# Kernel optimization log

Hardware: AMD Instinct MI355X
Metric: run time of the kernel (lower is better)

The kernel has to match this reference:

```python
import jax, jax.numpy as jnp
import numpy as np

B, S, D, H, E, K = 4, 4096, 256, 1024, 8, 2


def setup_inputs() -> dict:
    key = jax.random.key(0)
    ks = jax.random.split(key, 7)
    sc = 0.02
    return {
        "x": jax.random.normal(ks[0], (B, S, D), dtype=jnp.float32),
        "w_router": jax.random.normal(ks[1], (D, E), dtype=jnp.float32) * sc,
        "b_router": jnp.zeros((E,), dtype=jnp.float32),
        "w1": jax.random.normal(ks[2], (E, D, H), dtype=jnp.float32) * sc,
        "b1": jnp.zeros((E, H), dtype=jnp.float32),
        "w2": jax.random.normal(ks[3], (E, H, D), dtype=jnp.float32) * sc,
        "b2": jnp.zeros((E, D), dtype=jnp.float32),
    }


def reference(x, w_router, b_router, w1, b1, w2, b2):
    # Router: softmax over experts, then top-k selection + renormalization
    router_logits = jnp.einsum("bsd,de->bse", x, w_router) + b_router
    router_probs = jax.nn.softmax(router_logits, axis=-1)            # [B,S,E]
    top_probs, top_idx = jax.lax.top_k(router_probs, K)               # [B,S,K]
    top_w = top_probs / jnp.sum(top_probs, axis=-1, keepdims=True)    # renorm

    # Combine weights per expert: sum_k one_hot(idx_k) * w_k  -> [B,S,E]
    combine = jnp.sum(jax.nn.one_hot(top_idx, E, dtype=x.dtype) * top_w[..., None], axis=-2)

    # Dense equivalent of the masked gather/scatter dispatch:
    # out[b,s] = sum_e combine[b,s,e] * Expert_e(x[b,s])
    h = jax.nn.gelu(jnp.einsum("bsd,edh->bseh", x, w1) + b1, approximate=False)  # [B,S,E,H]
    y = jnp.einsum("bseh,ehd->bsed", h, w2) + b2                                  # [B,S,E,D]
    out = jnp.einsum("bsed,bse->bsd", y, combine)                                  # [B,S,D]
    return out, router_probs
```

## Files before the change

kernel.cpp:

```cpp
#include <hip/hip_runtime.h>

typedef float f32x4 __attribute__((ext_vector_type(4)));
typedef short s16x8 __attribute__((ext_vector_type(8)));

static constexpr int NTOK = 16384;
static constexpr int D    = 256;
static constexpr int H    = 1024;
static constexpr int E    = 8;

__device__ __forceinline__ float bf2f(unsigned short u) {
    return __uint_as_float(((unsigned int)u) << 16);
}
__device__ __forceinline__ unsigned short f2bf(float f) {
    unsigned int u = __float_as_uint(f);
    u += 0x7FFFu + ((u >> 16) & 1u);
    return (unsigned short)(u >> 16);
}
__device__ __forceinline__ s16x8 pack8(float4 a, float4 b) {
    s16x8 v;
    v[0] = (short)f2bf(a.x); v[1] = (short)f2bf(a.y);
    v[2] = (short)f2bf(a.z); v[3] = (short)f2bf(a.w);
    v[4] = (short)f2bf(b.x); v[5] = (short)f2bf(b.y);
    v[6] = (short)f2bf(b.z); v[7] = (short)f2bf(b.w);
    return v;
}

__global__ void __launch_bounds__(256) convert_kernel(
    const float* __restrict__ w1, const float* __restrict__ w2,
    unsigned short* __restrict__ w1t, unsigned short* __restrict__ w2t)
{
    __shared__ unsigned short tile[32][33];
    int b = blockIdx.x;
    const float* src; unsigned short* dst;
    int Rr, Cc, tr, tc;
    if (b < 2048) {
        int e = b >> 8, tt = b & 255;
        Rr = 256; Cc = 1024; tr = tt >> 5; tc = tt & 31;
        src = w1 + (size_t)e * Rr * Cc; dst = w1t + (size_t)e * Rr * Cc;
    } else {
        b -= 2048;
        int e = b >> 8, tt = b & 255;
        Rr = 1024; Cc = 256; tr = tt >> 3; tc = tt & 7;
        src = w2 + (size_t)e * Rr * Cc; dst = w2t + (size_t)e * Rr * Cc;
    }
    const int tid = threadIdx.x;
    const int c = tid & 31, r0 = tid >> 5;
    #pragma unroll
    for (int rr = 0; rr < 32; rr += 8)
        tile[r0 + rr][c] = f2bf(src[(size_t)(tr * 32 + r0 + rr) * Cc + tc * 32 + c]);
    __syncthreads();
    #pragma unroll
    for (int rr = 0; rr < 32; rr += 8)
        dst[(size_t)(tc * 32 + r0 + rr) * Rr + tr * 32 + c] = tile[c][r0 + rr];
}

__global__ void __launch_bounds__(1024) router_kernel(
    const float* __restrict__ x,
    const float* __restrict__ wr,
    const float* __restrict__ br,
    float* __restrict__ probs_out,
    int* __restrict__ cnt, int* __restrict__ list, float* __restrict__ wlist)
{
    __shared__ float wrs[D][9];
    __shared__ int lcnt[8];
    __shared__ int gbase[8];
    const int tid = threadIdx.x;
    if (tid < 256) {
        float4 a = *reinterpret_cast<const float4*>(wr + tid * 8);
        float4 b = *reinterpret_cast<const float4*>(wr + tid * 8 + 4);
        wrs[tid][0] = a.x; wrs[tid][1] = a.y; wrs[tid][2] = a.z; wrs[tid][3] = a.w;
        wrs[tid][4] = b.x; wrs[tid][5] = b.y; wrs[tid][6] = b.z; wrs[tid][7] = b.w;
    }
    if (tid < 8) lcnt[tid] = 0;
    __syncthreads();

    const int g = tid >> 4, l = tid & 15;
    const int t = blockIdx.x * 64 + g;

    float lg[8];
    #pragma unroll
    for (int e = 0; e < 8; ++e) lg[e] = 0.f;

    const float* xr = x + (size_t)t * D;
    #pragma unroll
    for (int r = 0; r < 4; ++r) {
        const int d = r * 64 + l * 4;
        float4 xv = *reinterpret_cast<const float4*>(xr + d);
        #pragma unroll
        for (int j = 0; j < 4; ++j) {
            const float xf = (j == 0) ? xv.x : (j == 1) ? xv.y : (j == 2) ? xv.z : xv.w;
            #pragma unroll
            for (int e = 0; e < 8; ++e) lg[e] += xf * wrs[d + j][e];
        }
    }
    #pragma unroll
    for (int off = 1; off < 16; off <<= 1)
        #pragma unroll
        for (int e = 0; e < 8; ++e) lg[e] += __shfl_xor(lg[e], off, 16);

    int i1 = 0, i2 = 0, lp1 = 0, lp2 = 0;
    float wa = 0.f, wb = 0.f;
    if (l == 0) {
        #pragma unroll
        for (int e = 0; e < 8; ++e) lg[e] += br[e];
        float mx = lg[0];
        #pragma unroll
        for (int e = 1; e < 8; ++e) mx = fmaxf(mx, lg[e]);
        float p[8], s = 0.f;
        #pragma unroll
        for (int e = 0; e < 8; ++e) { p[e] = expf(lg[e] - mx); s += p[e]; }
        const float inv = 1.f / s;
        #pragma unroll
        for (int e = 0; e < 8; ++e) p[e] *= inv;
        float4 o0 = {p[0], p[1], p[2], p[3]}, o1 = {p[4], p[5], p[6], p[7]};
        *reinterpret_cast<float4*>(probs_out + t * 8)     = o0;
        *reinterpret_cast<float4*>(probs_out + t * 8 + 4) = o1;

        #pragma unroll
        for (int e = 1; e < 8; ++e) if (p[e] > p[i1]) i1 = e;
        i2 = (i1 == 0) ? 1 : 0;
        #pragma unroll
        for (int e = 0; e < 8; ++e) if (e != i1 && p[e] > p[i2]) i2 = e;
        const float sw = p[i1] + p[i2];
        wa = p[i1] / sw; wb = p[i2] / sw;
        lp1 = atomicAdd(&lcnt[i1], 1);
        lp2 = atomicAdd(&lcnt[i2], 1);
    }
    __syncthreads();
    if (tid < 8) gbase[tid] = atomicAdd(&cnt[tid], lcnt[tid]);
    __syncthreads();
    if (l == 0) {
        int pos = gbase[i1] + lp1;
        list[i1 * NTOK + pos] = t;
        wlist[i1 * NTOK + pos] = wa;
        pos = gbase[i2] + lp2;
        list[i2 * NTOK + pos] = t | (1 << 30);
        wlist[i2 * NTOK + pos] = wb;
    }
}

__global__ void __launch_bounds__(512, 4) expert_kernel_v5(
    const float* __restrict__ x,
    const unsigned short* __restrict__ w1t,
    const unsigned short* __restrict__ w2t,
    const float* __restrict__ b1,
    const float* __restrict__ b2,
    const int* __restrict__ cnt, const int* __restrict__ list,
    const float* __restrict__ wlist,
    float* __restrict__ out,
    float* __restrict__ ybuf32,
    unsigned short* __restrict__ ybuf16,
    const int mode)
{
    const int e = blockIdx.y;
    int n = cnt[e]; n = (n < 0) ? 0 : ((n > NTOK) ? NTOK : n);
    const int tile0 = blockIdx.x * 64;
    if (tile0 >= n) return;
    const int nvalid = (n - tile0 < 64) ? (n - tile0) : 64;

    __shared__ __align__(16) unsigned short W1s[2][32 * 264];
    __shared__ __align__(16) unsigned short W2s[2][256 * 32];
    __shared__ __align__(16) unsigned short Hs [2][64 * 40];
    __shared__ int   toks[64];
    __shared__ float wgts[64];

    const int tid  = threadIdx.x;
    const int lane = tid & 63;
    const int wv   = tid >> 6;
    const int mrow = lane & 15;
    const int kb   = lane >> 4;
    const int key4 = (mrow & 3) ^ ((mrow >> 2) & 3);
    const int rb    = wv & 3;
    const int chb   = wv >> 2;
    const int tpart = wv & 1;
    const int dpart = wv >> 1;

    if (tid < 64) {
        if (tid < nvalid) {
            toks[tid] = list[e * NTOK + tile0 + tid];
            wgts[tid] = wlist[e * NTOK + tile0 + tid];
        } else { toks[tid] = 0; wgts[tid] = 0.f; }
    }

    const size_t w1b = (size_t)e * H * D;
    const size_t w2b = (size_t)e * D * H;
    s16x8 pfW1[2], pfW2[2];

    #define LOADW1(HC)                                                                  \
        _Pragma("unroll")                                                               \
        for (int k = 0; k < 2; ++k) {                                                   \
            const int s = k * 512 + tid, h1 = s >> 5, c1 = s & 31;                      \
            pfW1[k] = *reinterpret_cast<const s16x8*>(                                  \
                w1t + w1b + (size_t)((HC) * 32 + h1) * D + c1 * 8);                     \
        }
    #define STOREW1(BUF)                                                                \
        _Pragma("unroll")                                                               \
        for (int k = 0; k < 2; ++k) {                                                   \
            const int s = k * 512 + tid, h1 = s >> 5, c1 = s & 31;                      \
            *reinterpret_cast<s16x8*>(&W1s[BUF][h1 * 264 + c1 * 8]) = pfW1[k];          \
        }
    #define LOADW2(HC)                                                                  \
        _Pragma("unroll")                                                               \
        for (int k = 0; k < 2; ++k) {                                                   \
            const int s = k * 512 + tid, d2 = s >> 2, c2 = s & 3;                       \
            pfW2[k] = *reinterpret_cast<const s16x8*>(                                  \
                w2t + w2b + (size_t)d2 * H + (HC) * 32 + c2 * 8);                       \
        }
    #define STOREW2(BUF)                                                                \
        _Pragma("unroll")                                                               \
        for (int k = 0; k < 2; ++k) {                                                   \
            const int s = k * 512 + tid, d2 = s >> 2, c2 = s & 3;                       \
            const int k2 = (d2 & 3) ^ ((d2 >> 2) & 3);                                  \
            *reinterpret_cast<s16x8*>(&W2s[BUF][d2 * 32 + ((c2 ^ k2) << 3)]) = pfW2[k]; \
        }

    LOADW1(0);
    __syncthreads();

    s16x8 aFrag[8];
    {
        const float* xrow = x + (size_t)(toks[rb * 16 + mrow] & 0x3FFF) * D;
        #pragma unroll
        for (int ks = 0; ks < 8; ++ks) {
            const float* src = xrow + ks * 32 + kb * 8;
            aFrag[ks] = pack8(*reinterpret_cast<const float4*>(src),
                              *reinterpret_cast<const float4*>(src + 4));
        }
    }

    STOREW1(0);
    LOADW1(1);
    LOADW2(0);
    __syncthreads();

    f32x4 accYt[2][4];
    #pragma unroll
    for (int i = 0; i < 2; ++i)
        #pragma unroll
        for (int j = 0; j < 4; ++j) accYt[i][j] = (f32x4){0.f, 0.f, 0.f, 0.f};

    for (int hc = 0; hc < 32; ++hc) {
        const int cur = hc & 1, nxt = cur ^ 1;

        if (hc < 31) { STOREW1(nxt); }
        if (hc < 30) { LOADW1(hc + 2); }
        STOREW2(cur);
        if (hc < 31) { LOADW2(hc + 1); }

        f32x4 accH = (f32x4){0.f, 0.f, 0.f, 0.f};
        {
            const int brow = chb * 16 + mrow;
            #pragma unroll
            for (int ks = 0; ks < 8; ++ks) {
                s16x8 bfrag = *reinterpret_cast<const s16x8*>(
                    &W1s[cur][brow * 264 + ks * 32 + kb * 8]);
                accH = __builtin_amdgcn_mfma_f32_16x16x32_bf16(aFrag[ks], bfrag, accH, 0, 0, 0);
            }
            const float bias = b1[e * H + hc * 32 + brow];
            #pragma unroll
            for (int r = 0; r < 4; ++r) {
                const int t = rb * 16 + kb * 4 + r;
                const float vvf = accH[r] + bias;
                const float g = 0.5f * vvf * (1.0f + erff(vvf * 0.70710678118654752f));
                Hs[cur][t * 40 + brow] = f2bf(g);
            }
        }

        if (hc > 0) {
            s16x8 bfrag[2];
            #pragma unroll
            for (int tg = 0; tg < 2; ++tg)
                bfrag[tg] = *reinterpret_cast<const s16x8*>(
                    &Hs[nxt][((tpart * 2 + tg) * 16 + mrow) * 40 + kb * 8]);
            #pragma unroll
            for (int db = 0; db < 4; ++db) {
                const int d = (dpart * 4 + db) * 16 + mrow;
                s16x8 afrag = *reinterpret_cast<const s16x8*>(
                    &W2s[nxt][d * 32 + ((kb ^ key4) << 3)]);
                #pragma unroll
                for (int tg = 0; tg < 2; ++tg)
                    accYt[tg][db] = __builtin_amdgcn_mfma_f32_16x16x32_bf16(
                        afrag, bfrag[tg], accYt[tg][db], 0, 0, 0);
            }
        }
        __syncthreads();
    }

    {
        s16x8 bfrag[2];
        #pragma unroll
        for (int tg = 0; tg < 2; ++tg)
            bfrag[tg] = *reinterpret_cast<const s16x8*>(
                &Hs[1][((tpart * 2 + tg) * 16 + mrow) * 40 + kb * 8]);
        #pragma unroll
        for (int db = 0; db < 4; ++db) {
            const int d = (dpart * 4 + db) * 16 + mrow;
            s16x8 afrag = *reinterpret_cast<const s16x8*>(
                &W2s[1][d * 32 + ((kb ^ key4) << 3)]);
            #pragma unroll
            for (int tg = 0; tg < 2; ++tg)
                accYt[tg][db] = __builtin_amdgcn_mfma_f32_16x16x32_bf16(
                    afrag, bfrag[tg], accYt[tg][db], 0, 0, 0);
        }
    }

    #pragma unroll
    for (int tg = 0; tg < 2; ++tg) {
        const int tloc = (tpart * 2 + tg) * 16 + mrow;
        if (tloc < nvalid) {
            const float wt = wgts[tloc];
            const int raw = toks[tloc];
            const int t = raw & 0x3FFF;
            const size_t slotbase = ((size_t)((raw >> 30) & 1) * NTOK + t) * D;
            if (mode == 1) {
                float* ybase = ybuf32 + slotbase;
                #pragma unroll
                for (int db = 0; db < 4; ++db) {
                    const int d0 = (dpart * 4 + db) * 16 + kb * 4;
                    const float4 bv = *reinterpret_cast<const float4*>(b2 + e * D + d0);
                    float4 v = {(accYt[tg][db][0] + bv.x) * wt, (accYt[tg][db][1] + bv.y) * wt,
                                (accYt[tg][db][2] + bv.z) * wt, (accYt[tg][db][3] + bv.w) * wt};
                    *reinterpret_cast<float4*>(ybase + d0) = v;
                }
            } else if (mode == 2) {
                unsigned short* ybase = ybuf16 + slotbase;
                #pragma unroll
                for (int db = 0; db < 4; ++db) {
                    const int d0 = (dpart * 4 + db) * 16 + kb * 4;
                    const float4 bv = *reinterpret_cast<const float4*>(b2 + e * D + d0);
                    ushort4 v;
                    v.x = f2bf((accYt[tg][db][0] + bv.x) * wt);
                    v.y = f2bf((accYt[tg][db][1] + bv.y) * wt);
                    v.z = f2bf((accYt[tg][db][2] + bv.z) * wt);
                    v.w = f2bf((accYt[tg][db][3] + bv.w) * wt);
                    *reinterpret_cast<ushort4*>(ybase + d0) = v;
                }
            } else {
                float* obase = out + (size_t)t * D;
                #pragma unroll
                for (int db = 0; db < 4; ++db) {
                    const int d0 = (dpart * 4 + db) * 16 + kb * 4;
                    const float4 bv = *reinterpret_cast<const float4*>(b2 + e * D + d0);
                    atomicAdd(obase + d0 + 0, (accYt[tg][db][0] + bv.x) * wt);
                    atomicAdd(obase + d0 + 1, (accYt[tg][db][1] + bv.y) * wt);
                    atomicAdd(obase + d0 + 2, (accYt[tg][db][2] + bv.z) * wt);
                    atomicAdd(obase + d0 + 3, (accYt[tg][db][3] + bv.w) * wt);
                }
            }
        }
    }
    #undef LOADW1
    #undef STOREW1
    #undef LOADW2
    #undef STOREW2
}

__global__ void __launch_bounds__(256) combine_f32_kernel(
    const float* __restrict__ ybuf, float* __restrict__ out)
{
    const size_t i = ((size_t)blockIdx.x * 256 + threadIdx.x) * 4;
    float4 a = *reinterpret_cast<const float4*>(ybuf + i);
    float4 b = *reinterpret_cast<const float4*>(ybuf + (size_t)NTOK * D + i);
    float4 v = {a.x + b.x, a.y + b.y, a.z + b.z, a.w + b.w};
    *reinterpret_cast<float4*>(out + i) = v;
}
__global__ void __launch_bounds__(256) combine_bf16_kernel(
    const unsigned short* __restrict__ ybuf, float* __restrict__ out)
{
    const size_t i = ((size_t)blockIdx.x * 256 + threadIdx.x) * 4;
    ushort4 a = *reinterpret_cast<const ushort4*>(ybuf + i);
    ushort4 b = *reinterpret_cast<const ushort4*>(ybuf + (size_t)NTOK * D + i);
    float4 v = {bf2f(a.x) + bf2f(b.x), bf2f(a.y) + bf2f(b.y),
                bf2f(a.z) + bf2f(b.z), bf2f(a.w) + bf2f(b.w)};
    *reinterpret_cast<float4*>(out + i) = v;
}

__global__ void __launch_bounds__(256) expert_kernel_fp32(
    const float* __restrict__ x, const float* __restrict__ w1, const float* __restrict__ w2,
    const float* __restrict__ b1, const float* __restrict__ b2,
    const int* __restrict__ cnt, const int* __restrict__ list, const float* __restrict__ wlist,
    float* __restrict__ out)
{
    const int e = blockIdx.y;
    int n = cnt[e]; n = (n < 0) ? 0 : ((n > NTOK) ? NTOK : n);
    const int tile0 = blockIdx.x * 64;
    if (tile0 >= n) return;
    const int nvalid = (n - tile0 < 64) ? (n - tile0) : 64;

    __shared__ __align__(16) unsigned short Xs [64 * 264];
    __shared__ __align__(16) unsigned short W1s[64 * 264];
    __shared__ __align__(16) unsigned short W2s[256 * 72];
    __shared__ __align__(16) unsigned short Hs [64 * 72];
    __shared__ int   toks[64];
    __shared__ float wgts[64];

    const int tid = threadIdx.x, lane = tid & 63, wv = tid >> 6;
    const int mrow = lane & 15, kb = lane >> 4;

    if (tid < 64) {
        if (tid < nvalid) {
            toks[tid] = list[e * NTOK + tile0 + tid] & 0x3FFF;
            wgts[tid] = wlist[e * NTOK + tile0 + tid];
        } else { toks[tid] = 0; wgts[tid] = 0.f; }
    }
    __syncthreads();

    #pragma unroll
    for (int r = 0; r < 8; ++r) {
        int v = r * 256 + tid, row = v >> 5, c8 = v & 31;
        s16x8 val = {0,0,0,0,0,0,0,0};
        if (row < nvalid) {
            const float* src = x + (size_t)toks[row] * D + c8 * 8;
            val = pack8(*reinterpret_cast<const float4*>(src),
                        *reinterpret_cast<const float4*>(src + 4));
        }
        *reinterpret_cast<s16x8*>(&Xs[row * 264 + c8 * 8]) = val;
    }

    f32x4 accYt[16];
    #pragma unroll
    for (int i = 0; i < 16; ++i) accYt[i] = (f32x4){0.f, 0.f, 0.f, 0.f};

    const int wr2 = wv >> 1, wc2 = wv & 1;
    const int hgrp = tid & 7, dblk = tid >> 3;
    const int dgrp = tid & 31, hblk8 = tid >> 5;

    for (int hc = 0; hc < 16; ++hc) {
        __syncthreads();
        {
            s16x8 Y8[8];
            #pragma unroll
            for (int i = 0; i < 8; ++i) {
                const float* src = w1 + ((size_t)(e * D + dblk * 8 + i)) * H + hc * 64 + hgrp * 8;
                Y8[i] = pack8(*reinterpret_cast<const float4*>(src),
                              *reinterpret_cast<const float4*>(src + 4));
            }
            #pragma unroll
            for (int j = 0; j < 8; ++j) {
                s16x8 V;
                #pragma unroll
                for (int i = 0; i < 8; ++i) V[i] = Y8[i][j];
                *reinterpret_cast<s16x8*>(&W1s[(hgrp * 8 + j) * 264 + dblk * 8]) = V;
            }
        }
        {
            s16x8 Z8[8];
            #pragma unroll
            for (int i = 0; i < 8; ++i) {
                const float* src = w2 + ((size_t)(e * H + hc * 64 + hblk8 * 8 + i)) * D + dgrp * 8;
                Z8[i] = pack8(*reinterpret_cast<const float4*>(src),
                              *reinterpret_cast<const float4*>(src + 4));
            }
            const int hswz = (hblk8 ^ (dgrp & 7)) << 3;
            #pragma unroll
            for (int j = 0; j < 8; ++j) {
                s16x8 V;
                #pragma unroll
                for (int i = 0; i < 8; ++i) V[i] = Z8[i][j];
                *reinterpret_cast<s16x8*>(&W2s[(dgrp * 8 + j) * 72 + hswz]) = V;
            }
        }
        __syncthreads();

        f32x4 accH[2][2];
        #pragma unroll
        for (int i = 0; i < 2; ++i)
            #pragma unroll
            for (int j = 0; j < 2; ++j) accH[i][j] = (f32x4){0.f, 0.f, 0.f, 0.f};
        #pragma unroll
        for (int ks = 0; ks < 8; ++ks) {
            const int koff = ks * 32 + kb * 8;
            s16x8 a0 = *reinterpret_cast<const s16x8*>(&Xs [((wr2*2+0)*16 + mrow)*264 + koff]);
            s16x8 a1 = *reinterpret_cast<const s16x8*>(&Xs [((wr2*2+1)*16 + mrow)*264 + koff]);
            s16x8 b0 = *reinterpret_cast<const s16x8*>(&W1s[((wc2*2+0)*16 + mrow)*264 + koff]);
            s16x8 b1v= *reinterpret_cast<const s16x8*>(&W1s[((wc2*2+1)*16 + mrow)*264 + koff]);
            accH[0][0] = __builtin_amdgcn_mfma_f32_16x16x32_bf16(a0, b0,  accH[0][0], 0, 0, 0);
            accH[0][1] = __builtin_amdgcn_mfma_f32_16x16x32_bf16(a0, b1v, accH[0][1], 0, 0, 0);
            accH[1][0] = __builtin_amdgcn_mfma_f32_16x16x32_bf16(a1, b0,  accH[1][0], 0, 0, 0);
            accH[1][1] = __builtin_amdgcn_mfma_f32_16x16x32_bf16(a1, b1v, accH[1][1], 0, 0, 0);
        }
        #pragma unroll
        for (int i = 0; i < 2; ++i)
            #pragma unroll
            for (int j = 0; j < 2; ++j) {
                const int hloc = (wc2*2 + j) * 16 + mrow;
                const float bias = b1[e * H + hc * 64 + hloc];
                #pragma unroll
                for (int r = 0; r < 4; ++r) {
                    const int m = (wr2*2 + i) * 16 + kb * 4 + r;
                    float vvf = accH[i][j][r] + bias;
                    float g = 0.5f * vvf * (1.0f + erff(vvf * 0.70710678118654752f));
                    Hs[m * 72 + hloc] = f2bf(g);
                }
            }
        __syncthreads();

        #pragma unroll
        for (int ks = 0; ks < 2; ++ks) {
            const int koff = ks * 32 + kb * 8;
            s16x8 bfrag = *reinterpret_cast<const s16x8*>(&Hs[(wv * 16 + mrow) * 72 + koff]);
            #pragma unroll
            for (int db = 0; db < 16; ++db) {
                const int arow = db * 16 + mrow;
                const int akey = (arow >> 3) & 7;
                s16x8 afrag = *reinterpret_cast<const s16x8*>(
                    &W2s[arow * 72 + (((ks * 4 + kb) ^ akey) << 3)]);
                accYt[db] = __builtin_amdgcn_mfma_f32_16x16x32_bf16(afrag, bfrag, accYt[db], 0, 0, 0);
            }
        }
    }

    {
        const int t = wv * 16 + mrow;
        if (t < nvalid) {
            const float wt = wgts[t];
            float* obase = out + (size_t)toks[t] * D;
            #pragma unroll
            for (int db = 0; db < 16; ++db) {
                const int d0 = db * 16 + kb * 4;
                #pragma unroll
                for (int r = 0; r < 4; ++r)
                    atomicAdd(obase + d0 + r, (accYt[db][r] + b2[e * D + d0 + r]) * wt);
            }
        }
    }
}

extern "C" void kernel_launch(void* const* d_in, const int* in_sizes, int n_in,
                              void* d_out, int out_size, void* d_ws, size_t ws_size,
                              hipStream_t stream)
{
    const float* x  = (const float*)d_in[0];
    const float* wr = (const float*)d_in[1];
    const float* br = (const float*)d_in[2];
    const float* w1 = (const float*)d_in[3];
    const float* b1 = (const float*)d_in[4];
    const float* w2 = (const float*)d_in[5];
    const float* b2 = (const float*)d_in[6];
    float* out = (float*)d_out;

    char* ws = (char*)d_ws;
    int*   cnt   = (int*)ws;
    int*   list  = (int*)(ws + 256);
    float* wlist = (float*)(ws + 524544);
    unsigned short* w1t = (unsigned short*)(ws + 1048832);
    unsigned short* w2t = (unsigned short*)(ws + 5243136);
    float*          ybuf32 = (float*)(ws + 9437440);
    unsigned short* ybuf16 = (unsigned short*)(ws + 9437440);

    const bool big = ws_size >= 9437440;
    int mode = 0;
    if (big) {
        if (ws_size >= 9437440ull + 33554432ull)      mode = 1;
        else if (ws_size >= 9437440ull + 16777216ull) mode = 2;
    }

    if (mode == 0)
        hipMemsetAsync(out, 0, (size_t)NTOK * D * 4, stream);
    hipMemsetAsync(cnt, 0, 256, stream);
    if (big)
        convert_kernel<<<4096, 256, 0, stream>>>(w1, w2, w1t, w2t);
    router_kernel<<<NTOK / 64, 1024, 0, stream>>>(x, wr, br, out + (size_t)NTOK * D, cnt, list, wlist);
    if (big) {
        expert_kernel_v5<<<dim3(256, 8), 512, 0, stream>>>(
            x, w1t, w2t, b1, b2, cnt, list, wlist, out, ybuf32, ybuf16, mode);
        if (mode == 1)
            combine_f32_kernel<<<(NTOK * D / 4) / 256, 256, 0, stream>>>(ybuf32, out);
        else if (mode == 2)
            combine_bf16_kernel<<<(NTOK * D / 4) / 256, 256, 0, stream>>>(ybuf16, out);
    } else {
        expert_kernel_fp32<<<dim3(256, 8), 256, 0, stream>>>(x, w1, w2, b1, b2, cnt, list, wlist, out);
    }
}
```

Baseline: 219.4 us.

## Fuse weight conversion with router, use tanh GELU approximation, lighter barrier

Merges the weight transpose/convert kernel and the router kernel into one launch, with block ranges split by blockIdx, so one kernel launch and its dependency gap go away. Replaces the exact erf GELU in the expert kernel with a tanh-form approximation built from __expf and a fast divide, which cuts transcendental cost but changes numerics relative to the exact-GELU reference. Swaps the per-iteration __syncthreads for a barrier that waits only on LDS counters, so outstanding global loads can stay in flight across the barrier. In the non-big fallback path the prep kernel also runs the conversion blocks, writing into w1t/w2t pointers that may not fit in the workspace.

```diff
diff --git a/kernel.cpp b/kernel.cpp
--- a/kernel.cpp
+++ b/kernel.cpp
@@ -25,121 +25,125 @@
     return v;
 }
 
-__global__ void __launch_bounds__(256) convert_kernel(
+__device__ __forceinline__ void barrier_lds_only() {
+    __asm__ __volatile__("s_waitcnt lgkmcnt(0)" ::: "memory");
+    __builtin_amdgcn_s_barrier();
+    __asm__ __volatile__("" ::: "memory");
+}
+
+__global__ void __launch_bounds__(256) prep_kernel(
     const float* __restrict__ w1, const float* __restrict__ w2,
-    unsigned short* __restrict__ w1t, unsigned short* __restrict__ w2t)
-{
-    __shared__ unsigned short tile[32][33];
-    int b = blockIdx.x;
-    const float* src; unsigned short* dst;
-    int Rr, Cc, tr, tc;
-    if (b < 2048) {
-        int e = b >> 8, tt = b & 255;
-        Rr = 256; Cc = 1024; tr = tt >> 5; tc = tt & 31;
-        src = w1 + (size_t)e * Rr * Cc; dst = w1t + (size_t)e * Rr * Cc;
-    } else {
-        b -= 2048;
-        int e = b >> 8, tt = b & 255;
-        Rr = 1024; Cc = 256; tr = tt >> 3; tc = tt & 7;
-        src = w2 + (size_t)e * Rr * Cc; dst = w2t + (size_t)e * Rr * Cc;
-    }
-    const int tid = threadIdx.x;
-    const int c = tid & 31, r0 = tid >> 5;
-    #pragma unroll
-    for (int rr = 0; rr < 32; rr += 8)
-        tile[r0 + rr][c] = f2bf(src[(size_t)(tr * 32 + r0 + rr) * Cc + tc * 32 + c]);
-    __syncthreads();
-    #pragma unroll
-    for (int rr = 0; rr < 32; rr += 8)
-        dst[(size_t)(tc * 32 + r0 + rr) * Rr + tr * 32 + c] = tile[c][r0 + rr];
-}
-
-__global__ void __launch_bounds__(1024) router_kernel(
-    const float* __restrict__ x,
-    const float* __restrict__ wr,
-    const float* __restrict__ br,
-    float* __restrict__ probs_out,
+    unsigned short* __restrict__ w1t, unsigned short* __restrict__ w2t,
+    const float* __restrict__ x, const float* __restrict__ wr,
+    const float* __restrict__ br, float* __restrict__ probs_out,
     int* __restrict__ cnt, int* __restrict__ list, float* __restrict__ wlist)
 {
-    __shared__ float wrs[D][9];
-    __shared__ int lcnt[8];
-    __shared__ int gbase[8];
+    __shared__ __align__(16) char smem[9280];
     const int tid = threadIdx.x;
-    if (tid < 256) {
-        float4 a = *reinterpret_cast<const float4*>(wr + tid * 8);
-        float4 b = *reinterpret_cast<const float4*>(wr + tid * 8 + 4);
-        wrs[tid][0] = a.x; wrs[tid][1] = a.y; wrs[tid][2] = a.z; wrs[tid][3] = a.w;
-        wrs[tid][4] = b.x; wrs[tid][5] = b.y; wrs[tid][6] = b.z; wrs[tid][7] = b.w;
-    }
-    if (tid < 8) lcnt[tid] = 0;
-    __syncthreads();
-
-    const int g = tid >> 4, l = tid & 15;
-    const int t = blockIdx.x * 64 + g;
-
-    float lg[8];
-    #pragma unroll
-    for (int e = 0; e < 8; ++e) lg[e] = 0.f;
-
-    const float* xr = x + (size_t)t * D;
-    #pragma unroll
-    for (int r = 0; r < 4; ++r) {
-        const int d = r * 64 + l * 4;
-        float4 xv = *reinterpret_cast<const float4*>(xr + d);
-        #pragma unroll
-        for (int j = 0; j < 4; ++j) {
-            const float xf = (j == 0) ? xv.x : (j == 1) ? xv.y : (j == 2) ? xv.z : xv.w;
-            #pragma unroll
-            for (int e = 0; e < 8; ++e) lg[e] += xf * wrs[d + j][e];
-        }
-    }
-    #pragma unroll
-    for (int off = 1; off < 16; off <<= 1)
-        #pragma unroll
-        for (int e = 0; e < 8; ++e) lg[e] += __shfl_xor(lg[e], off, 16);
-
-    int i1 = 0, i2 = 0, lp1 = 0, lp2 = 0;
-    float wa = 0.f, wb = 0.f;
-    if (l == 0) {
-        #pragma unroll
-        for (int e = 0; e < 8; ++e) lg[e] += br[e];
-        float mx = lg[0];
-        #pragma unroll
-        for (int e = 1; e < 8; ++e) mx = fmaxf(mx, lg[e]);
-        float p[8], s = 0.f;
-        #pragma unroll
-        for (int e = 0; e < 8; ++e) { p[e] = expf(lg[e] - mx); s += p[e]; }
-        const float inv = 1.f / s;
-        #pragma unroll
-        for (int e = 0; e < 8; ++e) p[e] *= inv;
-        float4 o0 = {p[0], p[1], p[2], p[3]}, o1 = {p[4], p[5], p[6], p[7]};
-        *reinterpret_cast<float4*>(probs_out + t * 8)     = o0;
-        *reinterpret_cast<float4*>(probs_out + t * 8 + 4) = o1;
-
-        #pragma unroll
-        for (int e = 1; e < 8; ++e) if (p[e] > p[i1]) i1 = e;
-        i2 = (i1 == 0) ? 1 : 0;
-        #pragma unroll
-        for (int e = 0; e < 8; ++e) if (e != i1 && p[e] > p[i2]) i2 = e;
-        const float sw = p[i1] + p[i2];
-        wa = p[i1] / sw; wb = p[i2] / sw;
-        lp1 = atomicAdd(&lcnt[i1], 1);
-        lp2 = atomicAdd(&lcnt[i2], 1);
-    }
-    __syncthreads();
-    if (tid < 8) gbase[tid] = atomicAdd(&cnt[tid], lcnt[tid]);
-    __syncthreads();
-    if (l == 0) {
-        int pos = gbase[i1] + lp1;
-        list[i1 * NTOK + pos] = t;
-        wlist[i1 * NTOK + pos] = wa;
-        pos = gbase[i2] + lp2;
-        list[i2 * NTOK + pos] = t | (1 << 30);
-        wlist[i2 * NTOK + pos] = wb;
-    }
-}
-
-__global__ void __launch_bounds__(512, 4) expert_kernel_v5(
+
+    if (blockIdx.x < 4096) {
+        unsigned short (*tile)[33] = reinterpret_cast<unsigned short(*)[33]>(smem);
+        int b = blockIdx.x;
+        const float* src; unsigned short* dst;
+        int Rr, Cc, tr, tc;
+        if (b < 2048) {
+            int e = b >> 8, tt = b & 255;
+            Rr = 256; Cc = 1024; tr = tt >> 5; tc = tt & 31;
+            src = w1 + (size_t)e * Rr * Cc; dst = w1t + (size_t)e * Rr * Cc;
+        } else {
+            b -= 2048;
+            int e = b >> 8, tt = b & 255;
+            Rr = 1024; Cc = 256; tr = tt >> 3; tc = tt & 7;
+            src = w2 + (size_t)e * Rr * Cc; dst = w2t + (size_t)e * Rr * Cc;
+        }
+        const int c = tid & 31, r0 = tid >> 5;
+        #pragma unroll
+        for (int rr = 0; rr < 32; rr += 8)
+            tile[r0 + rr][c] = f2bf(src[(size_t)(tr * 32 + r0 + rr) * Cc + tc * 32 + c]);
+        __syncthreads();
+        #pragma unroll
+        for (int rr = 0; rr < 32; rr += 8)
+            dst[(size_t)(tc * 32 + r0 + rr) * Rr + tr * 32 + c] = tile[c][r0 + rr];
+    } else {
+        float (*wrs)[9] = reinterpret_cast<float(*)[9]>(smem);
+        int* lcnt  = reinterpret_cast<int*>(smem + 9216);
+        int* gbase = lcnt + 8;
+
+        if (tid < 8) lcnt[tid] = 0;
+        {
+            float4 a = *reinterpret_cast<const float4*>(wr + tid * 8);
+            float4 b = *reinterpret_cast<const float4*>(wr + tid * 8 + 4);
+            wrs[tid][0] = a.x; wrs[tid][1] = a.y; wrs[tid][2] = a.z; wrs[tid][3] = a.w;
+            wrs[tid][4] = b.x; wrs[tid][5] = b.y; wrs[tid][6] = b.z; wrs[tid][7] = b.w;
+        }
+        __syncthreads();
+
+        const int g = tid >> 4, l = tid & 15;
+        const int t = (blockIdx.x - 4096) * 16 + g;
+
+        float lg[8];
+        #pragma unroll
+        for (int e = 0; e < 8; ++e) lg[e] = 0.f;
+        const float* xr = x + (size_t)t * D;
+        #pragma unroll
+        for (int r = 0; r < 4; ++r) {
+            const int d = r * 64 + l * 4;
+            float4 xv = *reinterpret_cast<const float4*>(xr + d);
+            #pragma unroll
+            for (int j = 0; j < 4; ++j) {
+                const float xf = (j == 0) ? xv.x : (j == 1) ? xv.y : (j == 2) ? xv.z : xv.w;
+                #pragma unroll
+                for (int e = 0; e < 8; ++e) lg[e] += xf * wrs[d + j][e];
+            }
+        }
+        #pragma unroll
+        for (int off = 1; off < 16; off <<= 1)
+            #pragma unroll
+            for (int e = 0; e < 8; ++e) lg[e] += __shfl_xor(lg[e], off, 16);
+
+        int i1 = 0, i2 = 0, lp1 = 0, lp2 = 0;
+        float wa = 0.f, wb = 0.f;
+        if (l == 0) {
+            #pragma unroll
+            for (int e = 0; e < 8; ++e) lg[e] += br[e];
+            float mx = lg[0];
+            #pragma unroll
+            for (int e = 1; e < 8; ++e) mx = fmaxf(mx, lg[e]);
+            float p[8], s = 0.f;
+            #pragma unroll
+            for (int e = 0; e < 8; ++e) { p[e] = expf(lg[e] - mx); s += p[e]; }
+            const float inv = 1.f / s;
+            #pragma unroll
+            for (int e = 0; e < 8; ++e) p[e] *= inv;
+            float4 o0 = {p[0], p[1], p[2], p[3]}, o1 = {p[4], p[5], p[6], p[7]};
+            *reinterpret_cast<float4*>(probs_out + t * 8)     = o0;
+            *reinterpret_cast<float4*>(probs_out + t * 8 + 4) = o1;
+
+            #pragma unroll
+            for (int e = 1; e < 8; ++e) if (p[e] > p[i1]) i1 = e;
+            i2 = (i1 == 0) ? 1 : 0;
+            #pragma unroll
+            for (int e = 0; e < 8; ++e) if (e != i1 && p[e] > p[i2]) i2 = e;
+            const float sw = p[i1] + p[i2];
+            wa = p[i1] / sw; wb = p[i2] / sw;
+            lp1 = atomicAdd(&lcnt[i1], 1);
+            lp2 = atomicAdd(&lcnt[i2], 1);
+        }
+        __syncthreads();
+        if (tid < 8) gbase[tid] = atomicAdd(&cnt[tid], lcnt[tid]);
+        __syncthreads();
+        if (l == 0) {
+            int pos = gbase[i1] + lp1;
+            list[i1 * NTOK + pos] = t;
+            wlist[i1 * NTOK + pos] = wa;
+            pos = gbase[i2] + lp2;
+            list[i2 * NTOK + pos] = t | (1 << 30);
+            wlist[i2 * NTOK + pos] = wb;
+        }
+    }
+}
+
+__global__ void __launch_bounds__(512, 4) expert_kernel_v6(
     const float* __restrict__ x,
     const unsigned short* __restrict__ w1t,
     const unsigned short* __restrict__ w2t,
@@ -260,8 +264,9 @@
             #pragma unroll
             for (int r = 0; r < 4; ++r) {
                 const int t = rb * 16 + kb * 4 + r;
-                const float vvf = accH[r] + bias;
-                const float g = 0.5f * vvf * (1.0f + erff(vvf * 0.70710678118654752f));
+                const float v = accH[r] + bias;
+                const float u = v * (0.7978845608f + 0.0356774081f * v * v);
+                const float g = __fdividef(v, 1.0f + __expf(-2.0f * u));
                 Hs[cur][t * 40 + brow] = f2bf(g);
             }
         }
@@ -283,7 +288,7 @@
                         afrag, bfrag[tg], accYt[tg][db], 0, 0, 0);
             }
         }
-        __syncthreads();
+        barrier_lds_only();
     }
 
     {
@@ -558,17 +563,18 @@
     if (mode == 0)
         hipMemsetAsync(out, 0, (size_t)NTOK * D * 4, stream);
     hipMemsetAsync(cnt, 0, 256, stream);
-    if (big)
-        convert_kernel<<<4096, 256, 0, stream>>>(w1, w2, w1t, w2t);
-    router_kernel<<<NTOK / 64, 1024, 0, stream>>>(x, wr, br, out + (size_t)NTOK * D, cnt, list, wlist);
     if (big) {
-        expert_kernel_v5<<<dim3(256, 8), 512, 0, stream>>>(
+        prep_kernel<<<5120, 256, 0, stream>>>(w1, w2, w1t, w2t,
+                                              x, wr, br, out + (size_t)NTOK * D, cnt, list, wlist);
+        expert_kernel_v6<<<dim3(256, 8), 512, 0, stream>>>(
             x, w1t, w2t, b1, b2, cnt, list, wlist, out, ybuf32, ybuf16, mode);
         if (mode == 1)
             combine_f32_kernel<<<(NTOK * D / 4) / 256, 256, 0, stream>>>(ybuf32, out);
         else if (mode == 2)
             combine_bf16_kernel<<<(NTOK * D / 4) / 256, 256, 0, stream>>>(ybuf16, out);
     } else {
+        prep_kernel<<<5120, 256, 0, stream>>>(w1, w2, w1t, w2t,
+                                              x, wr, br, out + (size_t)NTOK * D, cnt, list, wlist);
         expert_kernel_fp32<<<dim3(256, 8), 256, 0, stream>>>(x, w1, w2, b1, b2, cnt, list, wlist, out);
     }
 }
```

Result: slower. 226.1 us (+3.1%).
